# Optimization experiments

Measured on AMD Instinct MI355X. Metric: run time of the kernel, lower is better.

## Reference

```python
import jax, jax.numpy as jnp
import numpy as np

EPS_BN = 1e-5
EPS_COS = 1e-8
M_BINS = 10


def _bn(x, g, b):
    # eval-mode BatchNorm2d with running_mean=0, running_var=1
    s = g / jnp.sqrt(1.0 + EPS_BN)
    return x * s[None, :, None, None] + b[None, :, None, None]


def _dw(x, w, pad, dil):
    # depthwise conv, x [B,C,H,W], w [C,1,kh,kw]
    return jax.lax.conv_general_dilated(
        x, w, window_strides=(1, 1), padding=pad, rhs_dilation=dil,
        dimension_numbers=('NCHW', 'OIHW', 'NCHW'),
        feature_group_count=x.shape[1])


def setup_inputs() -> dict:
    key = jax.random.key(0)
    ks = jax.random.split(key, 20)
    B, INP, OUP, H, W = 16, 64, 64, 128, 128
    f32 = jnp.float32
    d = {}
    d['x'] = jax.random.normal(ks[0], (B, INP, H, W), f32)
    d['w_conv1'] = jax.random.normal(ks[1], (OUP, INP), f32) * 0.05
    d['pr_w1'] = jax.random.normal(ks[2], (OUP, 1, 1, 5), f32) * 0.2
    d['pr_w2'] = jax.random.normal(ks[3], (OUP, 1, 5, 1), f32) * 0.2
    d['pr_w3'] = jax.random.normal(ks[4], (OUP, 1, 1, 5), f32) * 0.2
    d['pr_w4'] = jax.random.normal(ks[5], (OUP, 1, 5, 1), f32) * 0.2
    d['pr_gamma'] = 1.0 + 0.1 * jax.random.normal(ks[6], (5, OUP), f32)
    d['pr_beta'] = 0.1 * jax.random.normal(ks[7], (5, OUP), f32)
    d['bn1_g'] = 1.0 + 0.1 * jax.random.normal(ks[8], (OUP,), f32)
    d['bn1_b'] = 0.1 * jax.random.normal(ks[9], (OUP,), f32)
    d['bn2_g'] = 1.0 + 0.1 * jax.random.normal(ks[10], (OUP,), f32)
    d['bn2_b'] = 0.1 * jax.random.normal(ks[11], (OUP,), f32)
    d['fc1_w'] = jax.random.normal(ks[12], (OUP, 2), f32) * 0.5
    d['fc1_b'] = 0.1 * jax.random.normal(ks[13], (OUP,), f32)
    d['phi1_w'] = jax.random.normal(ks[14], (OUP, OUP), f32) * 0.1
    d['phi1_b'] = 0.01 * jax.random.normal(ks[15], (OUP,), f32)
    d['phi2_w'] = jax.random.normal(ks[16], (OUP, OUP), f32) * 0.1
    d['phi2_b'] = 0.01 * jax.random.normal(ks[17], (OUP,), f32)
    d['phi3_w'] = jax.random.normal(ks[18], (OUP, OUP), f32) * 0.1
    d['phi3_b'] = 0.01 * jax.random.normal(ks[19], (OUP,), f32)
    d['w_conv2'] = jax.random.normal(jax.random.fold_in(key, 99), (OUP, 1), f32) * 0.1
    return d


def reference(x, w_conv1, pr_w1, pr_w2, pr_w3, pr_w4, pr_gamma, pr_beta,
              bn1_g, bn1_b, bn2_g, bn2_b, fc1_w, fc1_b,
              phi1_w, phi1_b, phi2_w, phi2_b, phi3_w, phi3_b, w_conv2):
    B, C, H, W = x.shape
    M = M_BINS
    OUP = w_conv1.shape[0]
    # conv1 (1x1) + Position_reinforcement branch
    x_c = jnp.einsum('oc,bchw->bohw', w_conv1, x)
    h = _bn(x_c, pr_gamma[0], pr_beta[0])
    h = _dw(h, pr_w1, ((0, 0), (2, 2)), (1, 1))
    h = _bn(h, pr_gamma[1], pr_beta[1])
    h = _dw(h, pr_w2, ((2, 2), (0, 0)), (1, 1))
    h = _bn(h, pr_gamma[2], pr_beta[2])
    h = _dw(h, pr_w3, ((0, 0), (4, 4)), (2, 2))
    h = _bn(h, pr_gamma[3], pr_beta[3])
    h = _dw(h, pr_w4, ((4, 4), (0, 0)), (2, 2))
    x_center = _bn(h, pr_gamma[4], pr_beta[4])
    # cosine similarity of each pixel feature with the global-avg feature
    g = jnp.mean(x, axis=(2, 3), keepdims=True)             # [B,C,1,1]
    num = jnp.sum(g * x, axis=1)                            # [B,H,W]
    gn = jnp.maximum(jnp.sqrt(jnp.sum(g * g, axis=1)), EPS_COS)
    xn = jnp.maximum(jnp.sqrt(jnp.sum(x * x, axis=1)), EPS_COS)
    S = num / (gn * xn)                                     # [B,H,W]
    Sf = S.reshape(B, H * W)
    # torch casts min/max with float() -> detached constants
    mn = jax.lax.stop_gradient(jnp.min(Sf, axis=1))
    mx = jax.lax.stop_gradient(jnp.max(Sf, axis=1))
    t = jnp.arange(M, dtype=x.dtype) / (M - 1)
    levels = mn[:, None] + (mx - mn)[:, None] * t[None, :]  # [B,M]
    diff = jnp.abs(levels[:, None, :] - Sf[:, :, None])     # [B,HW,M] soft bins
    V = jnp.where(diff < 0.5 / M, 1.0 - diff, jnp.zeros((), x.dtype))
    colsum = jnp.sum(V, axis=1)                             # [B,M]
    # torch normalizes by V.sum() while only columns 0..j are filled -> cumsum
    denom = jnp.cumsum(colsum, axis=1)
    Ch = jnp.stack([colsum / denom, levels], axis=-1)       # [B,M,2]
    Cf = Ch.reshape(-1, 2) @ fc1_w.T + fc1_b                # [B*M,OUP]
    Cq = Cf.reshape(B, OUP, M)                              # raw view as in torch
    p1 = jnp.einsum('oc,bcm->bom', phi1_w, Cq) + phi1_b[None, :, None]
    p2 = jnp.einsum('oc,bcm->bom', phi2_w, Cq) + phi2_b[None, :, None]
    X = jax.nn.softmax(jnp.einsum('bcm,bcn->bmn', p1, p2), axis=-1)  # [B,M,M]
    p3 = jnp.einsum('oc,bcm->bom', phi3_w, Cq) + phi3_b[None, :, None]
    Lp = jnp.einsum('bcm,bmn->bcn', p3, X)                  # [B,OUP,M]
    Vr = V.reshape(B, M, H * W)                             # raw view as in torch
    R = jnp.einsum('bcm,bmk->bck', Lp, Vr).reshape(B, OUP, H, W)
    x_tex = _bn(R, bn1_g, bn1_b)
    x_full = _bn(w_conv2[:, 0][None, :, None, None] * S[:, None, :, :], bn2_g, bn2_b)
    att = jax.nn.sigmoid(x_full + x_tex + x_center)
    return x * att
```

## Files before the change

### kernel.cpp

```cpp
#include <hip/hip_runtime.h>
#include <hip/hip_bf16.h>
#include <math.h>

#define NB   16
#define NC   64
#define NH   128
#define NW   128
#define NHW  16384
#define NM   10
#define XCS  16416

__global__ __launch_bounds__(256) void k_gmean(const float* __restrict__ x,
                                               double* __restrict__ g) {
    int bc = blockIdx.x;
    const float* xp = x + (size_t)bc * NHW;
    double s = 0.0;
    for (int i = threadIdx.x; i < NHW / 4; i += 256) {
        float4 v = ((const float4*)xp)[i];
        s += (double)v.x + (double)v.y + (double)v.z + (double)v.w;
    }
    for (int off = 32; off; off >>= 1) s += __shfl_down(s, off);
    __shared__ double red[4];
    int wid = threadIdx.x >> 6, lane = threadIdx.x & 63;
    if (lane == 0) red[wid] = s;
    __syncthreads();
    if (threadIdx.x == 0)
        g[bc] = (red[0] + red[1] + red[2] + red[3]) * (1.0 / (double)NHW);
}

__global__ __launch_bounds__(256) void k_misc(const float* __restrict__ W,
                                              const double* __restrict__ g,
                                              float* __restrict__ Wt,
                                              double* __restrict__ gn) {
    if (blockIdx.x == 0) {
        for (int e = threadIdx.x; e < 64 * 64; e += 256) {
            int c = e >> 6, o = e & 63;
            Wt[c * 64 + o] = W[o * 64 + c];
        }
    } else if (threadIdx.x == 0) {
        int b = blockIdx.x - 1;
        const double* gb = g + b * NC;
        double gsq = 0.0;
        for (int c = 0; c < NC; ++c) gsq += gb[c] * gb[c];
        gn[b] = fmax(sqrt(gsq), 1e-8);
    }
}

__global__ __launch_bounds__(256, 4) void k_conv1_S(
        const float* __restrict__ x, const float* __restrict__ Wt,
        const double* __restrict__ g, const double* __restrict__ gn,
        float* __restrict__ xc, double* __restrict__ S,
        double* __restrict__ pmn, double* __restrict__ pmx) {
    int bid = blockIdx.x;
    int P = bid * 256 + threadIdx.x;
    int b = P >> 14, k = P & (NHW - 1);
    const float* xb = x + (size_t)b * NC * NHW + k;

    float xv[NC];
#pragma unroll
    for (int c = 0; c < NC; ++c) xv[c] = xb[(size_t)c * NHW];

    double Sv;
    {
        const double* gb = g + b * NC;
        double num = 0.0, sq = 0.0;
#pragma unroll
        for (int c = 0; c < NC; ++c) {
            double v = (double)xv[c];
            num += gb[c] * v;
            sq  += v * v;
        }
        double xn = fmax(sqrt(sq), 1e-8);
        Sv = num / (gn[b] * xn);
        S[P] = Sv;
    }

    {
        double mn = Sv, mx = Sv;
        for (int off = 32; off; off >>= 1) {
            mn = fmin(mn, __shfl_down(mn, off));
            mx = fmax(mx, __shfl_down(mx, off));
        }
        __shared__ double rmn[4], rmx[4];
        int wid = threadIdx.x >> 6, lane = threadIdx.x & 63;
        if (lane == 0) { rmn[wid] = mn; rmx[wid] = mx; }
        __syncthreads();
        if (threadIdx.x == 0) {
            pmn[bid] = fmin(fmin(rmn[0], rmn[1]), fmin(rmn[2], rmn[3]));
            pmx[bid] = fmax(fmax(rmx[0], rmx[1]), fmax(rmx[2], rmx[3]));
        }
    }

    float* xcb = xc + (size_t)b * NC * XCS + k;
    for (int p = 0; p < 4; ++p) {
        int o0 = p * 16;
        float acc[16];
#pragma unroll
        for (int j = 0; j < 16; ++j) acc[j] = 0.f;
#pragma unroll
        for (int c = 0; c < NC; ++c) {
            const float* wr = Wt + c * 64 + o0;
#pragma unroll
            for (int j = 0; j < 16; ++j)
                acc[j] = fmaf(wr[j], xv[c], acc[j]);
        }
#pragma unroll
        for (int j = 0; j < 16; ++j)
            xcb[(size_t)(o0 + j) * XCS] = acc[j];
    }
}

__global__ __launch_bounds__(256) void k_hist(const double* __restrict__ S,
                                              const double* __restrict__ pmn,
                                              const double* __restrict__ pmx,
                                              double* __restrict__ pbins) {
    int blk = blockIdx.x, b = blk >> 2, part = blk & 3;
    int tid = threadIdx.x;
    __shared__ double sa, sz;
    if (tid < 64) {
        double mn = pmn[(b << 6) + tid], mx = pmx[(b << 6) + tid];
        for (int off = 32; off; off >>= 1) {
            mn = fmin(mn, __shfl_down(mn, off));
            mx = fmax(mx, __shfl_down(mx, off));
        }
        if (tid == 0) { sa = mn; sz = mx; }
    }
    __syncthreads();
    double a = sa, z = sz;
    double lv[NM];
#pragma unroll
    for (int m = 0; m < NM; ++m) lv[m] = a + (z - a) * ((double)m / 9.0);

    const double* Sb = S + (size_t)b * NHW + part * 4096;
    double bins[NM];
#pragma unroll
    for (int m = 0; m < NM; ++m) bins[m] = 0.0;
    for (int i = tid; i < 4096; i += 256) {
        double v = Sb[i];
#pragma unroll
        for (int m = 0; m < NM; ++m) {
            double d = fabs(lv[m] - v);
            if (d < 0.05) bins[m] += 1.0 - d;
        }
    }
#pragma unroll
    for (int m = 0; m < NM; ++m)
        for (int off = 32; off; off >>= 1) bins[m] += __shfl_down(bins[m], off);
    __shared__ double wb[4][NM];
    int wid = tid >> 6, lane = tid & 63;
    if (lane == 0) {
#pragma unroll
        for (int m = 0; m < NM; ++m) wb[wid][m] = bins[m];
    }
    __syncthreads();
    if (tid == 0) {
#pragma unroll
        for (int m = 0; m < NM; ++m)
            pbins[blk * NM + m] = wb[0][m] + wb[1][m] + wb[2][m] + wb[3][m];
    }
}

__global__ __launch_bounds__(256) void k_chain(
        const double* __restrict__ pmn, const double* __restrict__ pmx,
        const double* __restrict__ pbins,
        const float* __restrict__ fc1w, const float* __restrict__ fc1b,
        const float* __restrict__ ph1w, const float* __restrict__ ph1b,
        const float* __restrict__ ph2w, const float* __restrict__ ph2b,
        const float* __restrict__ ph3w, const float* __restrict__ ph3b,
        double* __restrict__ levelsOut, float* __restrict__ LpOut) {
    int b = blockIdx.x, tid = threadIdx.x;
    __shared__ double sa, sz;
    if (tid < 64) {
        double mn = pmn[(b << 6) + tid], mx = pmx[(b << 6) + tid];
        for (int off = 32; off; off >>= 1) {
            mn = fmin(mn, __shfl_down(mn, off));
            mx = fmax(mx, __shfl_down(mx, off));
        }
        if (tid == 0) { sa = mn; sz = mx; }
    }
    __syncthreads();
    __shared__ double levS[NM];
    __shared__ float ratio[NM];
    if (tid == 0) {
        double a = sa, z = sz;
        for (int m = 0; m < NM; ++m) levS[m] = a + (z - a) * ((double)m / 9.0);
        double den = 0.0;
        for (int m = 0; m < NM; ++m) {
            double cs = ((pbins[(4*b)*NM+m] + pbins[(4*b+1)*NM+m])
                        + pbins[(4*b+2)*NM+m]) + pbins[(4*b+3)*NM+m];
            den += cs;
            ratio[m] = (float)(cs / den);
        }
    }
    __syncthreads();

    __shared__ float CfL[640];
    for (int idx = tid; idx < 640; idx += 256) {
        int rm = idx >> 6, o = idx & 63;
        CfL[idx] = ratio[rm] * fc1w[o*2+0] + (float)levS[rm] * fc1w[o*2+1] + fc1b[o];
    }
    __syncthreads();

    __shared__ float P1[640], P2[640], P3[640];
    for (int idx = tid; idx < 640; idx += 256) {
        int o = idx / 10, m = idx - o * 10;
        float a1 = ph1b[o], a2 = ph2b[o], a3 = ph3b[o];
        for (int c2 = 0; c2 < NC; ++c2) {
            float cq = CfL[c2*10 + m];
            a1 = fmaf(ph1w[o*NC + c2], cq, a1);
            a2 = fmaf(ph2w[o*NC + c2], cq, a2);
            a3 = fmaf(ph3w[o*NC + c2], cq, a3);
        }
        P1[idx] = a1; P2[idx] = a2; P3[idx] = a3;
    }
    __syncthreads();

    __shared__ float XL[100];
    if (tid < 100) {
        int m = tid / 10, n = tid - (tid/10)*10;
        float acc = 0.f;
        for (int c2 = 0; c2 < NC; ++c2)
            acc = fmaf(P1[c2*10 + m], P2[c2*10 + n], acc);
        XL[tid] = acc;
    }
    __syncthreads();
    if (tid < NM) {
        float mxr = XL[tid*10];
        for (int n = 1; n < NM; ++n) mxr = fmaxf(mxr, XL[tid*10 + n]);
        float e[NM], sum = 0.f;
        for (int n = 0; n < NM; ++n) { e[n] = expf(XL[tid*10+n] - mxr); sum += e[n]; }
        for (int n = 0; n < NM; ++n) XL[tid*10+n] = e[n] / sum;
    }
    __syncthreads();

    for (int idx = tid; idx < 640; idx += 256) {
        int c2 = idx / 10, n = idx - (idx/10)*10;
        float acc = 0.f;
#pragma unroll
        for (int m = 0; m < NM; ++m) acc = fmaf(P3[c2*10 + m], XL[m*10 + n], acc);
        LpOut[b*640 + idx] = acc;
    }
    if (tid < NM) levelsOut[b*NM + tid] = levS[tid];
}

__global__ __launch_bounds__(256) void k_vgath(
        const double* __restrict__ S, const double* __restrict__ levels,
        float* __restrict__ vg, float* __restrict__ Sf) {
    int P = blockIdx.x * 256 + threadIdx.x;
    int b = P >> 14, k = P & (NHW - 1);
    __shared__ double levL[NM];
    if (threadIdx.x < NM) levL[threadIdx.x] = levels[b*NM + threadIdx.x];
    __syncthreads();
    const double* Sb = S + (size_t)b * NHW;
    float* vgb = vg + (size_t)b * NM * NHW;
#pragma unroll
    for (int i = 0; i < NM; ++i) {
        int j = i * NHW + k;
        int p = j / 10;
        int m = j - p * 10;
        double d = fabs(levL[m] - Sb[p]);
        vgb[i * NHW + k] = (d < 0.05) ? (float)(1.0 - d) : 0.f;
    }
    Sf[P] = (float)Sb[k];
}

__global__ __launch_bounds__(256) void k_dwfinal(
        const float* __restrict__ xc, const float* __restrict__ x,
        const float* __restrict__ vg, const float* __restrict__ Sf,
        const float* __restrict__ Lp,
        const float* __restrict__ pw1, const float* __restrict__ pw2,
        const float* __restrict__ pw3, const float* __restrict__ pw4,
        const float* __restrict__ gamma, const float* __restrict__ beta,
        const float* __restrict__ bn1g, const float* __restrict__ bn1b,
        const float* __restrict__ bn2g, const float* __restrict__ bn2b,
        const float* __restrict__ wconv2, float* __restrict__ out) {
    int tile = blockIdx.x, c = blockIdx.y, b = blockIdx.z;
    int R0 = (tile >> 1) * 32, C0 = (tile & 1) * 64;
    const float inv = 0.9999950000374997f;
    float s0 = gamma[0*NC+c]*inv, b0 = beta[0*NC+c];
    float s1 = gamma[1*NC+c]*inv, b1 = beta[1*NC+c];
    float s2 = gamma[2*NC+c]*inv, b2 = beta[2*NC+c];
    float s3 = gamma[3*NC+c]*inv, b3 = beta[3*NC+c];
    float s4 = gamma[4*NC+c]*inv, b4 = beta[4*NC+c];
    float w1[5], w2[5], w3[5], w4[5];
#pragma unroll
    for (int q = 0; q < 5; ++q) {
        w1[q] = pw1[c*5+q]; w2[q] = pw2[c*5+q];
        w3[q] = pw3[c*5+q]; w4[q] = pw4[c*5+q];
    }
    float Ac = wconv2[c] * (bn2g[c] * inv);
    float Bc = bn2b[c] + bn1b[c];
    float S1 = bn1g[c] * inv;

    __shared__ __align__(16) float A[44*76];
    __shared__ __align__(16) float Bf[44*72];
    __shared__ float LpL[NM];
    const float* src = xc + (size_t)(b*NC + c) * XCS;
    int tid = threadIdx.x;

    if (tid < NM) LpL[tid] = Lp[b*640 + c*10 + tid];

    for (int t = tid; t < 44*19; t += 256) {
        int r = t / 19, g2 = t - r*19;
        int gy = R0 - 6 + r, gx0 = C0 - 6 + 4*g2;
        float4 v = make_float4(0.f, 0.f, 0.f, 0.f);
        bool rowOK = (unsigned)gy < NH;
        if (rowOK) {
            const float* rowp = src + gy*NW;
            if ((unsigned)gx0 <= (unsigned)(NW-4)) {
                v = *(const float4*)(rowp + gx0);
            } else {
                float* pv = (float*)&v;
#pragma unroll
                for (int u = 0; u < 4; ++u) {
                    int gx = gx0 + u;
                    if ((unsigned)gx < NW) pv[u] = rowp[gx];
                }
            }
        }
        float4 w;
        w.x = (rowOK && (unsigned)(gx0+0) < NW) ? fmaf(v.x, s0, b0) : 0.f;
        w.y = (rowOK && (unsigned)(gx0+1) < NW) ? fmaf(v.y, s0, b0) : 0.f;
        w.z = (rowOK && (unsigned)(gx0+2) < NW) ? fmaf(v.z, s0, b0) : 0.f;
        w.w = (rowOK && (unsigned)(gx0+3) < NW) ? fmaf(v.w, s0, b0) : 0.f;
        *(float4*)&A[r*76 + 4*g2] = w;
    }
    __syncthreads();

    for (int t = tid; t < 44*18; t += 256) {
        int r = t / 18, g2 = t - r*18;
        float xw[8];
        *(float4*)&xw[0] = *(float4*)&A[r*76 + 4*g2];
        *(float4*)&xw[4] = *(float4*)&A[r*76 + 4*g2 + 4];
        int gy = R0 - 6 + r;
        bool rowOK = (unsigned)gy < NH;
        float o[4];
#pragma unroll
        for (int u = 0; u < 4; ++u) {
            float acc = 0.f;
#pragma unroll
            for (int q = 0; q < 5; ++q) acc = fmaf(w1[q], xw[u+q], acc);
            int gx = C0 - 4 + 4*g2 + u;
            o[u] = (rowOK && (unsigned)gx < NW) ? fmaf(acc, s1, b1) : 0.f;
        }
        *(float4*)&Bf[r*72 + 4*g2] = *(float4*)o;
    }
    __syncthreads();

    for (int t = tid; t < 40*18; t += 256) {
        int r = t / 18, g2 = t - r*18;
        float ys[5][4];
#pragma unroll
        for (int p = 0; p < 5; ++p)
            *(float4*)&ys[p][0] = *(float4*)&Bf[(r+p)*72 + 4*g2];
        int gy = R0 - 4 + r;
        bool rowOK = (unsigned)gy < NH;
        float o[4];
#pragma unroll
        for (int u = 0; u < 4; ++u) {
            float acc = 0.f;
#pragma unroll
            for (int p = 0; p < 5; ++p) acc = fmaf(w2[p], ys[p][u], acc);
            int gx = C0 - 4 + 4*g2 + u;
            o[u] = (rowOK && (unsigned)gx < NW) ? fmaf(acc, s2, b2) : 0.f;
        }
        *(float4*)&A[r*72 + 4*g2] = *(float4*)o;
    }
    __syncthreads();

    for (int t = tid; t < 40*16; t += 256) {
        int r = t >> 4, g2 = t & 15;
        float xw[12];
        *(float4*)&xw[0] = *(float4*)&A[r*72 + 4*g2];
        *(float4*)&xw[4] = *(float4*)&A[r*72 + 4*g2 + 4];
        *(float4*)&xw[8] = *(float4*)&A[r*72 + 4*g2 + 8];
        int gy = R0 - 4 + r;
        bool rowOK = (unsigned)gy < NH;
        float o[4];
#pragma unroll
        for (int u = 0; u < 4; ++u) {
            float acc = 0.f;
#pragma unroll
            for (int q = 0; q < 5; ++q) acc = fmaf(w3[q], xw[u+2*q], acc);
            o[u] = rowOK ? fmaf(acc, s3, b3) : 0.f;
        }
        *(float4*)&Bf[r*64 + 4*g2] = *(float4*)o;
    }
    __syncthreads();

    const float* vgb = vg + (size_t)b * NM * NHW;
    const float* Sfb = Sf + (size_t)b * NHW;
    for (int t = tid; t < 32*16; t += 256) {
        int r = t >> 4, g2 = t & 15;
        float ys[5][4];
#pragma unroll
        for (int p = 0; p < 5; ++p)
            *(float4*)&ys[p][0] = *(float4*)&Bf[(r+2*p)*64 + 4*g2];
        int kbase = (R0 + r) * NW + C0 + 4*g2;
        size_t xbase = (size_t)(b*NC + c) * NHW + kbase;
        float4 xv = *(const float4*)&x[xbase];
        float4 skv = *(const float4*)&Sfb[kbase];
        const float* xvp = (const float*)&xv;
        const float* skp = (const float*)&skv;
        float vr[NM][4];
#pragma unroll
        for (int i = 0; i < NM; ++i)
            *(float4*)&vr[i][0] = *(const float4*)&vgb[i * NHW + kbase];
        float res[4];
#pragma unroll
        for (int u = 0; u < 4; ++u) {
            float acc = 0.f;
#pragma unroll
            for (int p = 0; p < 5; ++p) acc = fmaf(w4[p], ys[p][u], acc);
            float xcen = fmaf(acc, s4, b4);
            float R = 0.f;
#pragma unroll
            for (int i = 0; i < NM; ++i) R = fmaf(LpL[i], vr[i][u], R);
            float pre = fmaf(Ac, skp[u], Bc) + S1 * R + xcen;
            float e = __expf(-pre);
            float att = __builtin_amdgcn_rcpf(1.0f + e);
            res[u] = xvp[u] * att;
        }
        *(float4*)&out[xbase] = *(float4*)res;
    }
}

extern "C" void kernel_launch(void* const* d_in, const int* in_sizes, int n_in,
                              void* d_out, int out_size, void* d_ws, size_t ws_size,
                              hipStream_t stream) {
    (void)in_sizes; (void)n_in; (void)out_size; (void)ws_size;
    const float* x      = (const float*)d_in[0];
    const float* wconv1 = (const float*)d_in[1];
    const float* pw1    = (const float*)d_in[2];
    const float* pw2    = (const float*)d_in[3];
    const float* pw3    = (const float*)d_in[4];
    const float* pw4    = (const float*)d_in[5];
    const float* pgam   = (const float*)d_in[6];
    const float* pbet   = (const float*)d_in[7];
    const float* bn1g   = (const float*)d_in[8];
    const float* bn1b   = (const float*)d_in[9];
    const float* bn2g   = (const float*)d_in[10];
    const float* bn2b   = (const float*)d_in[11];
    const float* fc1w   = (const float*)d_in[12];
    const float* fc1b   = (const float*)d_in[13];
    const float* ph1w   = (const float*)d_in[14];
    const float* ph1b   = (const float*)d_in[15];
    const float* ph2w   = (const float*)d_in[16];
    const float* ph2b   = (const float*)d_in[17];
    const float* ph3w   = (const float*)d_in[18];
    const float* ph3b   = (const float*)d_in[19];
    const float* wconv2 = (const float*)d_in[20];
    float* out = (float*)d_out;

    float*  ws    = (float*)d_ws;
    float*  xc    = ws;
    double* Sd    = (double*)(ws + 1024 * XCS);
    double* g     = Sd + NB * NHW;
    double* lev   = g + NB * NC;
    double* gn    = lev + NB * NM;
    double* pmn   = gn + NB;
    double* pmx   = pmn + 1024;
    double* pbins = pmx + 1024;
    float*  Lp    = (float*)(pbins + 640);
    float*  vg    = Lp + NB * 640;
    float*  Sf    = vg + NB * NM * NHW;
    float*  Wt    = Sf + NB * NHW;

    k_gmean<<<NB * NC, 256, 0, stream>>>(x, g);
    k_misc<<<17, 256, 0, stream>>>(wconv1, g, Wt, gn);
    k_conv1_S<<<NB * NHW / 256, 256, 0, stream>>>(x, Wt, g, gn, xc, Sd,
                                                  pmn, pmx);
    k_hist<<<NB * 4, 256, 0, stream>>>(Sd, pmn, pmx, pbins);
    k_chain<<<NB, 256, 0, stream>>>(pmn, pmx, pbins, fc1w, fc1b,
                                    ph1w, ph1b, ph2w, ph2b, ph3w, ph3b,
                                    lev, Lp);
    k_vgath<<<NB * NHW / 256, 256, 0, stream>>>(Sd, lev, vg, Sf);
    k_dwfinal<<<dim3(8, NC, NB), 256, 0, stream>>>(
        xc, x, vg, Sf, Lp, pw1, pw2, pw3, pw4, pgam, pbet,
        bn1g, bn1b, bn2g, bn2b, wconv2, out);
}
```

Before: 163.2 us.

## Split fused conv1/cosine kernel into separate S and conv kernels

The fused kernel held all 64 channel values per pixel in registers, which limited occupancy. It is split into a cosine-similarity kernel that streams channels with four partial accumulators, and a 1x1 conv kernel whose grid gains a y dimension over four 16-output groups. This lowers register pressure and adds parallelism, but x is now read five times instead of once (about 4x64MB of extra traffic). The final sigmoid also switches from fast exp and reciprocal intrinsics to precise expf and division.

Measured after the change: 173.2 us. 6.1% more time.

```diff
diff --git a/kernel.cpp b/kernel.cpp
--- a/kernel.cpp
+++ b/kernel.cpp
@@ -46,68 +46,73 @@
     }
 }
 
-__global__ __launch_bounds__(256, 4) void k_conv1_S(
-        const float* __restrict__ x, const float* __restrict__ Wt,
-        const double* __restrict__ g, const double* __restrict__ gn,
-        float* __restrict__ xc, double* __restrict__ S,
+__global__ __launch_bounds__(256) void k_S(
+        const float* __restrict__ x, const double* __restrict__ g,
+        const double* __restrict__ gn, double* __restrict__ S,
         double* __restrict__ pmn, double* __restrict__ pmx) {
     int bid = blockIdx.x;
     int P = bid * 256 + threadIdx.x;
     int b = P >> 14, k = P & (NHW - 1);
     const float* xb = x + (size_t)b * NC * NHW + k;
-
-    float xv[NC];
-#pragma unroll
-    for (int c = 0; c < NC; ++c) xv[c] = xb[(size_t)c * NHW];
-
-    double Sv;
-    {
-        const double* gb = g + b * NC;
-        double num = 0.0, sq = 0.0;
-#pragma unroll
-        for (int c = 0; c < NC; ++c) {
-            double v = (double)xv[c];
-            num += gb[c] * v;
-            sq  += v * v;
-        }
-        double xn = fmax(sqrt(sq), 1e-8);
-        Sv = num / (gn[b] * xn);
-        S[P] = Sv;
-    }
-
-    {
-        double mn = Sv, mx = Sv;
-        for (int off = 32; off; off >>= 1) {
-            mn = fmin(mn, __shfl_down(mn, off));
-            mx = fmax(mx, __shfl_down(mx, off));
-        }
-        __shared__ double rmn[4], rmx[4];
-        int wid = threadIdx.x >> 6, lane = threadIdx.x & 63;
-        if (lane == 0) { rmn[wid] = mn; rmx[wid] = mx; }
-        __syncthreads();
-        if (threadIdx.x == 0) {
-            pmn[bid] = fmin(fmin(rmn[0], rmn[1]), fmin(rmn[2], rmn[3]));
-            pmx[bid] = fmax(fmax(rmx[0], rmx[1]), fmax(rmx[2], rmx[3]));
-        }
-    }
-
+    const double* gb = g + b * NC;
+
+    double n0 = 0.0, n1 = 0.0, n2 = 0.0, n3 = 0.0;
+    double q0 = 0.0, q1 = 0.0, q2 = 0.0, q3 = 0.0;
+#pragma unroll 4
+    for (int c = 0; c < NC; c += 4) {
+        double v0 = (double)xb[(size_t)(c+0) * NHW];
+        double v1 = (double)xb[(size_t)(c+1) * NHW];
+        double v2 = (double)xb[(size_t)(c+2) * NHW];
+        double v3 = (double)xb[(size_t)(c+3) * NHW];
+        n0 += gb[c+0] * v0;  q0 += v0 * v0;
+        n1 += gb[c+1] * v1;  q1 += v1 * v1;
+        n2 += gb[c+2] * v2;  q2 += v2 * v2;
+        n3 += gb[c+3] * v3;  q3 += v3 * v3;
+    }
+    double num = (n0 + n1) + (n2 + n3);
+    double sq  = (q0 + q1) + (q2 + q3);
+    double xn = fmax(sqrt(sq), 1e-8);
+    double Sv = num / (gn[b] * xn);
+    S[P] = Sv;
+
+    double mn = Sv, mx = Sv;
+    for (int off = 32; off; off >>= 1) {
+        mn = fmin(mn, __shfl_down(mn, off));
+        mx = fmax(mx, __shfl_down(mx, off));
+    }
+    __shared__ double rmn[4], rmx[4];
+    int wid = threadIdx.x >> 6, lane = threadIdx.x & 63;
+    if (lane == 0) { rmn[wid] = mn; rmx[wid] = mx; }
+    __syncthreads();
+    if (threadIdx.x == 0) {
+        pmn[bid] = fmin(fmin(rmn[0], rmn[1]), fmin(rmn[2], rmn[3]));
+        pmx[bid] = fmax(fmax(rmx[0], rmx[1]), fmax(rmx[2], rmx[3]));
+    }
+}
+
+__global__ __launch_bounds__(256) void k_conv(
+        const float* __restrict__ x, const float* __restrict__ Wt,
+        float* __restrict__ xc) {
+    int o0 = blockIdx.y * 16;
+    int P = blockIdx.x * 256 + threadIdx.x;
+    int b = P >> 14, k = P & (NHW - 1);
+    const float* xb = x + (size_t)b * NC * NHW + k;
+
+    float acc[16];
+#pragma unroll
+    for (int j = 0; j < 16; ++j) acc[j] = 0.f;
+#pragma unroll 8
+    for (int c = 0; c < NC; ++c) {
+        float v = xb[(size_t)c * NHW];
+        const float* wr = Wt + c * 64 + o0;
+#pragma unroll
+        for (int j = 0; j < 16; ++j)
+            acc[j] = fmaf(wr[j], v, acc[j]);
+    }
     float* xcb = xc + (size_t)b * NC * XCS + k;
-    for (int p = 0; p < 4; ++p) {
-        int o0 = p * 16;
-        float acc[16];
-#pragma unroll
-        for (int j = 0; j < 16; ++j) acc[j] = 0.f;
-#pragma unroll
-        for (int c = 0; c < NC; ++c) {
-            const float* wr = Wt + c * 64 + o0;
-#pragma unroll
-            for (int j = 0; j < 16; ++j)
-                acc[j] = fmaf(wr[j], xv[c], acc[j]);
-        }
-#pragma unroll
-        for (int j = 0; j < 16; ++j)
-            xcb[(size_t)(o0 + j) * XCS] = acc[j];
-    }
+#pragma unroll
+    for (int j = 0; j < 16; ++j)
+        xcb[(size_t)(o0 + j) * XCS] = acc[j];
 }
 
 __global__ __launch_bounds__(256) void k_hist(const double* __restrict__ S,
@@ -417,8 +422,7 @@
 #pragma unroll
             for (int i = 0; i < NM; ++i) R = fmaf(LpL[i], vr[i][u], R);
             float pre = fmaf(Ac, skp[u], Bc) + S1 * R + xcen;
-            float e = __expf(-pre);
-            float att = __builtin_amdgcn_rcpf(1.0f + e);
+            float att = 1.0f / (1.0f + expf(-pre));
             res[u] = xvp[u] * att;
         }
         *(float4*)&out[xbase] = *(float4*)res;
@@ -468,8 +472,8 @@
 
     k_gmean<<<NB * NC, 256, 0, stream>>>(x, g);
     k_misc<<<17, 256, 0, stream>>>(wconv1, g, Wt, gn);
-    k_conv1_S<<<NB * NHW / 256, 256, 0, stream>>>(x, Wt, g, gn, xc, Sd,
-                                                  pmn, pmx);
+    k_S<<<NB * NHW / 256, 256, 0, stream>>>(x, g, gn, Sd, pmn, pmx);
+    k_conv<<<dim3(NB * NHW / 256, 4), 256, 0, stream>>>(x, Wt, xc);
     k_hist<<<NB * 4, 256, 0, stream>>>(Sd, pmn, pmx, pbins);
     k_chain<<<NB, 256, 0, stream>>>(pmn, pmx, pbins, fc1w, fc1b,
                                     ph1w, ph1b, ph2w, ph2b, ph3w, ph3b,
```
